# Kernel tuning notes

Measured on AMD Instinct MI355X. Metric: run time of the kernel, lower is better.

Reference implementation:

```python
import jax, jax.numpy as jnp
import numpy as np

B, L, D_IN, H, TAGS = 16, 128, 512, 256, 45


def setup_inputs() -> dict:
    key = jax.random.key(0)
    ks = jax.random.split(key, 10)
    s = 0.02
    return {
        "contextualized": jax.random.normal(ks[0], (B, L, D_IN), jnp.float32),
        "sentence_lengths": jax.random.randint(ks[1], (B,), 64, L + 1, jnp.int32),
        "desired_arcs": jax.random.randint(ks[2], (B, L), 0, L + 1, jnp.int32),
        "desired_labels": jax.random.randint(ks[3], (B, L), 0, TAGS, jnp.int32),
        "W1": jax.random.normal(ks[4], (D_IN, H), jnp.float32) * s,
        "b1": jnp.zeros((H,), jnp.float32),
        "root": jax.random.normal(ks[5], (H,), jnp.float32) * s,
        "Wp": jax.random.normal(ks[6], (2 * H, H), jnp.float32) * s,
        "bp": jnp.zeros((H,), jnp.float32),
        "W_arc": jax.random.normal(ks[7], (H, 1), jnp.float32) * s,
        "b_arc": jnp.zeros((1,), jnp.float32),
        "W_lab": jax.random.normal(ks[8], (H, TAGS), jnp.float32) * s,
        "b_lab": jnp.zeros((TAGS,), jnp.float32),
    }


def _forward(contextualized, sentence_lengths, desired_arcs, desired_labels,
             W1, b1, root, Wp, bp, W_arc, b_arc, W_lab, b_lab):
    b, l, _ = contextualized.shape
    h = W1.shape[1]
    # token representations: dense + relu
    hidden = jax.nn.relu(contextualized @ W1 + b1)                      # [B,L,H]
    # prepend learned root vector
    root_t = jnp.broadcast_to(root, (b, 1, h))
    cwr = jnp.concatenate([root_t, hidden], axis=1)                     # [B,L+1,H]
    # pairs dense: concat([tile_a, tile_b]) @ Wp == hidden@Wa + cwr@Wb (broadcast-add)
    Wa, Wb = Wp[:h], Wp[h:]
    pre = (hidden @ Wa)[:, :, None, :] + (cwr @ Wb)[:, None, :, :] + bp
    pairs_repr = jax.nn.relu(pre)                                       # [B,L,L+1,H]
    # valid-token mask from sentence lengths
    mask = (jnp.arange(l)[None, :] < sentence_lengths[:, None]).astype(jnp.float32)
    denom = jnp.maximum(mask.sum(), 1.0)
    # UAS: arc logits over L+1 head candidates, softmax CE vs gold arcs
    arc_logits = jnp.squeeze(pairs_repr @ W_arc, -1) + b_arc[0]         # [B,L,L+1]
    arc_logp = jax.nn.log_softmax(arc_logits, axis=-1)
    arc_ce = -jnp.take_along_axis(arc_logp, desired_arcs[:, :, None], axis=-1)[..., 0]
    uas_loss = jnp.sum(arc_ce * mask) / denom
    # LAS: select pair repr at gold arc, dense -> tag logits, softmax CE
    sel = jnp.take_along_axis(pairs_repr, desired_arcs[:, :, None, None].astype(jnp.int32)
                              .repeat(1, axis=2), axis=2)[:, :, 0, :]   # [B,L,H]
    label_logits = sel @ W_lab + b_lab                                  # [B,L,TAGS]
    lab_logp = jax.nn.log_softmax(label_logits, axis=-1)
    lab_ce = -jnp.take_along_axis(lab_logp, desired_labels[:, :, None], axis=-1)[..., 0]
    las_loss = jnp.sum(lab_ce * mask) / denom
    return (uas_loss + las_loss) * 0.5


def reference(contextualized, sentence_lengths, desired_arcs, desired_labels,
              W1, b1, root, Wp, bp, W_arc, b_arc, W_lab, b_lab):
    return _forward(contextualized, sentence_lengths, desired_arcs, desired_labels,
                    W1, b1, root, Wp, bp, W_arc, b_arc, W_lab, b_lab)
```

## Files before the change

### kernel.cpp

```cpp
#include <hip/hip_runtime.h>
#include <math.h>

#define NB 16
#define NL 128
#define DIN 512
#define NH 256
#define NTAGS 45
#define NM (NB*NL)
#define NJ (NL+1)

#define H_OFF     0
#define U_OFF     (2*NM*NH)
#define HV_OFF    (3*NM*NH)
#define VROOT_OFF (4*NM*NH)
#define ACC_OFF   (VROOT_OFF + NH)

__global__ __launch_bounds__(256) void gemm_hidden(
    const float* __restrict__ A,
    const float* __restrict__ W,
    const float* __restrict__ Wp,
    const float* __restrict__ root,
    float* __restrict__ h,
    float* __restrict__ vroot,
    float* __restrict__ accum)
{
    __shared__ float As[2][16][36];
    __shared__ float Bs[2][16][68];
    __shared__ float part[4][64];
    int m0 = blockIdx.x * 32;
    int n0 = blockIdx.y * 64;
    int kbase = blockIdx.z * 256;
    int tid = threadIdx.x;
    if (blockIdx.x == 0 && blockIdx.y == 0 && blockIdx.z == 0 && tid == 0) {
        accum[0] = 0.f;
        ((int*)accum)[1] = 0;
    }
    int lm = tid >> 2, lk = (tid & 3) * 4;
    int bk = tid >> 4, bn = (tid & 15) * 4;
    int tm = tid >> 4, tn = tid & 15;
    float acc[2][4] = {{0.f}};
    float4 a_r, b_r;

    auto LOADK = [&](int c) {
        int k0 = kbase + c * 16;
        if (tid < 128)
            a_r = *(const float4*)&A[(size_t)(m0 + lm) * DIN + k0 + lk];
        b_r = *(const float4*)&W[(size_t)(k0 + bk) * NH + n0 + bn];
    };
    auto WRITE = [&](int buf) {
        if (tid < 128) {
            As[buf][lk + 0][lm] = a_r.x; As[buf][lk + 1][lm] = a_r.y;
            As[buf][lk + 2][lm] = a_r.z; As[buf][lk + 3][lm] = a_r.w;
        }
        *(float4*)&Bs[buf][bk][bn] = b_r;
    };

    LOADK(0);
    WRITE(0);
    LOADK(1);
    __syncthreads();
    for (int c = 0; c < 16; ++c) {
        int buf = c & 1;
        #pragma unroll
        for (int kk = 0; kk < 16; kk++) {
            float2 a2 = *(const float2*)&As[buf][kk][tm * 2];
            float4 bv = *(const float4*)&Bs[buf][kk][tn * 4];
            float ar[2] = {a2.x, a2.y};
            float br[4] = {bv.x, bv.y, bv.z, bv.w};
            #pragma unroll
            for (int r = 0; r < 2; r++)
                #pragma unroll
                for (int cc = 0; cc < 4; cc++)
                    acc[r][cc] = fmaf(ar[r], br[cc], acc[r][cc]);
        }
        if (c < 15) {
            WRITE(buf ^ 1);
            if (c < 14) LOADK(c + 2);
            __syncthreads();
        }
    }
    float* hz = h + (size_t)blockIdx.z * NM * NH;
    int col = n0 + tn * 4;
    #pragma unroll
    for (int r = 0; r < 2; r++) {
        int row = m0 + tm * 2 + r;
        *(float4*)&hz[(size_t)row * NH + col] =
            make_float4(acc[r][0], acc[r][1], acc[r][2], acc[r][3]);
    }

    if (blockIdx.x == 63 && blockIdx.z == 1) {
        __syncthreads();
        int vcol = n0 + (tid & 63);
        int kc = tid >> 6;
        float p = 0.f;
        #pragma unroll 8
        for (int c = kc * 64; c < kc * 64 + 64; c++)
            p += root[c] * Wp[(size_t)(NH + c) * NH + vcol];
        part[kc][tid & 63] = p;
        __syncthreads();
        if (tid < 64)
            vroot[n0 + tid] = part[0][tid] + part[1][tid]
                            + part[2][tid] + part[3][tid];
    }
}

__global__ __launch_bounds__(256) void gemm_uv(
    const float* __restrict__ h,
    const float* __restrict__ b1,
    const float* __restrict__ Wp,
    const float* __restrict__ bp,
    float* __restrict__ u,
    float* __restrict__ hv)
{
    __shared__ float As[2][16][68];
    __shared__ float Bs[2][16][36];
    int m0 = blockIdx.x * 64;
    int n0 = blockIdx.y * 32;
    int tid = threadIdx.x;
    bool isU = (n0 < NH);
    int arow = tid >> 2, akq = (tid & 3) * 4;
    int bk = tid >> 3, bn = (tid & 7) * 4;
    int tm = tid >> 3, tn = tid & 7;
    float acc[2][4] = {{0.f}};
    float4 ha_r, hb_r, bi_r, b_r;

    auto LOADK = [&](int c) {
        int k0 = c * 16;
        size_t base = (size_t)(m0 + arow) * NH + k0 + akq;
        ha_r = *(const float4*)&h[base];
        hb_r = *(const float4*)&h[base + (size_t)NM * NH];
        bi_r = *(const float4*)&b1[k0 + akq];
        if (tid < 128) {
            int ck = k0 + bk;
            if (isU) b_r = *(const float4*)&Wp[(size_t)ck * NH + n0 + bn];
            else     b_r = *(const float4*)&Wp[(size_t)(NH + ck) * NH + (n0 - NH) + bn];
        }
    };
    auto WRITE = [&](int buf) {
        As[buf][akq + 0][arow] = fmaxf(ha_r.x + hb_r.x + bi_r.x, 0.f);
        As[buf][akq + 1][arow] = fmaxf(ha_r.y + hb_r.y + bi_r.y, 0.f);
        As[buf][akq + 2][arow] = fmaxf(ha_r.z + hb_r.z + bi_r.z, 0.f);
        As[buf][akq + 3][arow] = fmaxf(ha_r.w + hb_r.w + bi_r.w, 0.f);
        if (tid < 128)
            *(float4*)&Bs[buf][bk][bn] = b_r;
    };

    LOADK(0);
    WRITE(0);
    LOADK(1);
    __syncthreads();
    for (int c = 0; c < 16; ++c) {
        int buf = c & 1;
        #pragma unroll
        for (int kk = 0; kk < 16; kk++) {
            float2 a2 = *(const float2*)&As[buf][kk][tm * 2];
            float4 bv = *(const float4*)&Bs[buf][kk][tn * 4];
            float ar[2] = {a2.x, a2.y};
            float br[4] = {bv.x, bv.y, bv.z, bv.w};
            #pragma unroll
            for (int r = 0; r < 2; r++)
                #pragma unroll
                for (int cc = 0; cc < 4; cc++)
                    acc[r][cc] = fmaf(ar[r], br[cc], acc[r][cc]);
        }
        if (c < 15) {
            WRITE(buf ^ 1);
            if (c < 14) LOADK(c + 2);
            __syncthreads();
        }
    }
    if (isU) {
        int col = n0 + tn * 4;
        float4 bb = *(const float4*)&bp[col];
        #pragma unroll
        for (int r = 0; r < 2; r++) {
            int row = m0 + tm * 2 + r;
            *(float4*)&u[(size_t)row * NH + col] = make_float4(
                acc[r][0] + bb.x, acc[r][1] + bb.y,
                acc[r][2] + bb.z, acc[r][3] + bb.w);
        }
    } else {
        int col = (n0 - NH) + tn * 4;
        #pragma unroll
        for (int r = 0; r < 2; r++) {
            int row = m0 + tm * 2 + r;
            *(float4*)&hv[(size_t)row * NH + col] = make_float4(
                acc[r][0], acc[r][1], acc[r][2], acc[r][3]);
        }
    }
}

#define NBLK (NB*16)

__global__ __launch_bounds__(512) void score_loss_kernel(
    const float* __restrict__ u, const float* __restrict__ hv,
    const float* __restrict__ vroot, const float* __restrict__ W_arc,
    const float* __restrict__ W_lab, const float* __restrict__ b_lab,
    const int* __restrict__ slens, const int* __restrict__ arcs,
    const int* __restrict__ labels,
    float* __restrict__ accum, float* __restrict__ out)
{
    __shared__ float2 v2_s[128][130];
    __shared__ float2 u2_s[8][128];
    __shared__ float2 wa2_s[128];
    __shared__ float2 sel2_s[32][9];
    __shared__ float  ce_s[8];
    __shared__ int    arc_s[8], lab_s[8];

    int bb = blockIdx.x;
    int i0 = blockIdx.y * 8;
    int tid = threadIdx.x;
    int w = tid >> 6;
    int lane = tid & 63;
    int slen = slens[bb];

    if (i0 < slen) {
        {
            int r = tid >> 6, kq = (tid & 63) * 4;
            float4 a4 = *(const float4*)&u[(size_t)(bb * NL + i0 + r) * NH + kq];
            u2_s[r][(kq >> 1) + 0] = make_float2(a4.x, a4.y);
            u2_s[r][(kq >> 1) + 1] = make_float2(a4.z, a4.w);
        }
        if (tid < 128)
            wa2_s[tid] = *(const float2*)&W_arc[tid * 2];
        if (tid < 8) {
            int rg = bb * NL + i0 + tid;
            arc_s[tid] = arcs[rg];
            lab_s[tid] = labels[rg];
        }

        {
            int jo  = lane >> 4;
            int kf0 = lane & 15;
            #pragma unroll
            for (int sj = 0; sj < 4; ++sj) {
                int j = sj * 32 + w * 4 + jo;
                const float* src = hv + (size_t)(bb * NL + j) * NH;
                #pragma unroll
                for (int sk = 0; sk < 4; ++sk) {
                    int kf = sk * 16 + kf0;
                    float4 t4 = *(const float4*)&src[kf * 4];
                    v2_s[2 * kf + 0][j + 1] = make_float2(t4.x, t4.y);
                    v2_s[2 * kf + 1][j + 1] = make_float2(t4.z, t4.w);
                }
            }
            if (w == 0) {
                float4 t4 = *(const float4*)&vroot[lane * 4];
                v2_s[2 * lane + 0][0] = make_float2(t4.x, t4.y);
                v2_s[2 * lane + 1][0] = make_float2(t4.z, t4.w);
            }
        }
        __syncthreads();

        float acc1 = 0.f, acc2 = 0.f, s128 = 0.f, lacc = 0.f;
        int a = arc_s[w];

        __builtin_amdgcn_s_setprio(1);
        #pragma unroll
        for (int c = 0; c < 4; ++c) {
            int k0 = c * 64;
            int kb = k0 >> 1;
            const float2* urow = u2_s[w] + kb;
            const float2* warow = wa2_s + kb;

            #pragma unroll 8
            for (int kk2 = 0; kk2 < 32; ++kk2) {
                float2 u2 = urow[kk2];
                float2 w2 = warow[kk2];
                float4 q = *(const float4*)&v2_s[kb + kk2][2 * lane];
                acc1 += fmaxf(u2.x + q.x, 0.f) * w2.x
                      + fmaxf(u2.y + q.y, 0.f) * w2.y;
                acc2 += fmaxf(u2.x + q.z, 0.f) * w2.x
                      + fmaxf(u2.y + q.w, 0.f) * w2.y;
            }
            if (lane < 32) {
                float2 u2 = urow[lane];
                float2 w2 = warow[lane];
                float2 vv = v2_s[kb + lane][128];
                s128 += fmaxf(u2.x + vv.x, 0.f) * w2.x
                      + fmaxf(u2.y + vv.y, 0.f) * w2.y;
                float2 vs = v2_s[kb + lane][a];
                sel2_s[lane][w] = make_float2(fmaxf(u2.x + vs.x, 0.f),
                                              fmaxf(u2.y + vs.y, 0.f));
            }
            if (lane < NTAGS) {
                #pragma unroll 8
                for (int kk2 = 0; kk2 < 32; ++kk2) {
                    float2 s2 = sel2_s[kk2][w];
                    float w0 = W_lab[(size_t)(k0 + 2 * kk2) * NTAGS + lane];
                    float w1 = W_lab[(size_t)(k0 + 2 * kk2 + 1) * NTAGS + lane];
                    lacc = fmaf(s2.x, w0, fmaf(s2.y, w1, lacc));
                }
            }
        }
        __builtin_amdgcn_s_setprio(0);

        float s128t = s128;
        #pragma unroll
        for (int off = 32; off > 0; off >>= 1)
            s128t += __shfl_xor(s128t, off);
        float m = fmaxf(acc1, acc2);
        #pragma unroll
        for (int off = 32; off > 0; off >>= 1)
            m = fmaxf(m, __shfl_xor(m, off));
        m = fmaxf(m, s128t);
        float e = expf(acc1 - m) + expf(acc2 - m);
        #pragma unroll
        for (int off = 32; off > 0; off >>= 1)
            e += __shfl_xor(e, off);
        e += expf(s128t - m);
        float cand = (a & 1) ? acc2 : acc1;
        float s_a = __shfl(cand, (a >> 1) & 63, 64);
        if (a == 128) s_a = s128t;
        float arc_ce = (m + logf(e)) - s_a;

        float logit = (lane < NTAGS) ? (lacc + b_lab[lane]) : -INFINITY;
        float m2 = logit;
        #pragma unroll
        for (int off = 32; off > 0; off >>= 1)
            m2 = fmaxf(m2, __shfl_xor(m2, off));
        float e2 = (lane < NTAGS) ? expf(logit - m2) : 0.f;
        #pragma unroll
        for (int off = 32; off > 0; off >>= 1)
            e2 += __shfl_xor(e2, off);
        float l_t = __shfl(logit, lab_s[w], 64);
        float lab_ce = (m2 + logf(e2)) - l_t;

        float tot = ((i0 + w) < slen) ? (arc_ce + lab_ce) : 0.f;
        if (lane == 0) ce_s[w] = tot;
        __syncthreads();
        if (tid == 0)
            atomicAdd(accum, ce_s[0] + ce_s[1] + ce_s[2] + ce_s[3]
                           + ce_s[4] + ce_s[5] + ce_s[6] + ce_s[7]);
    }

    if (tid == 0) {
        __threadfence();
        int prev = atomicAdd((int*)accum + 1, 1);
        if (prev == NBLK - 1) {
            int d = 0;
            #pragma unroll
            for (int q = 0; q < NB; ++q) d += slens[q];
            float s = atomicAdd(accum, 0.f);
            out[0] = 0.5f * s / fmaxf((float)d, 1.f);
        }
    }
}

extern "C" void kernel_launch(void* const* d_in, const int* in_sizes, int n_in,
                              void* d_out, int out_size, void* d_ws, size_t ws_size,
                              hipStream_t stream) {
    (void)in_sizes; (void)n_in; (void)out_size; (void)ws_size;
    const float* ctx   = (const float*)d_in[0];
    const int*   slens = (const int*)  d_in[1];
    const int*   arcs  = (const int*)  d_in[2];
    const int*   labs  = (const int*)  d_in[3];
    const float* W1    = (const float*)d_in[4];
    const float* b1    = (const float*)d_in[5];
    const float* root  = (const float*)d_in[6];
    const float* Wp    = (const float*)d_in[7];
    const float* bp    = (const float*)d_in[8];
    const float* W_arc = (const float*)d_in[9];
    const float* W_lab = (const float*)d_in[11];
    const float* b_lab = (const float*)d_in[12];
    float* out = (float*)d_out;

    float* ws    = (float*)d_ws;
    float* h     = ws + H_OFF;
    float* u     = ws + U_OFF;
    float* hv    = ws + HV_OFF;
    float* vroot = ws + VROOT_OFF;
    float* accum = ws + ACC_OFF;

    gemm_hidden<<<dim3(64, 4, 2), 256, 0, stream>>>(ctx, W1, Wp, root, h, vroot, accum);
    gemm_uv<<<dim3(32, 16), 256, 0, stream>>>(h, b1, Wp, bp, u, hv);
    score_loss_kernel<<<dim3(NB, 16), 512, 0, stream>>>(
        u, hv, vroot, W_arc, W_lab, b_lab, slens, arcs, labs, accum, out);
}
```

Baseline: 128.3 us.

## Split hidden-dim reduction across two wave groups in score kernel

```diff
diff --git a/kernel.cpp b/kernel.cpp
--- a/kernel.cpp
+++ b/kernel.cpp
@@ -192,7 +192,7 @@
 
 #define NBLK (NB*16)
 
-__global__ __launch_bounds__(512) void score_loss_kernel(
+__global__ __launch_bounds__(1024) void score_loss_kernel(
     const float* __restrict__ u, const float* __restrict__ hv,
     const float* __restrict__ vroot, const float* __restrict__ W_arc,
     const float* __restrict__ W_lab, const float* __restrict__ b_lab,
@@ -203,23 +203,26 @@
     __shared__ float2 v2_s[128][130];
     __shared__ float2 u2_s[8][128];
     __shared__ float2 wa2_s[128];
-    __shared__ float2 sel2_s[32][9];
+    __shared__ float2 sel2_s[32][17];
+    __shared__ float4 pair_s[8][64];
     __shared__ float  ce_s[8];
     __shared__ int    arc_s[8], lab_s[8];
 
     int bb = blockIdx.x;
     int i0 = blockIdx.y * 8;
     int tid = threadIdx.x;
-    int w = tid >> 6;
+    int w16 = tid >> 6;
     int lane = tid & 63;
+    int r  = w16 & 7;
+    int kh = w16 >> 3;
     int slen = slens[bb];
 
     if (i0 < slen) {
-        {
-            int r = tid >> 6, kq = (tid & 63) * 4;
-            float4 a4 = *(const float4*)&u[(size_t)(bb * NL + i0 + r) * NH + kq];
-            u2_s[r][(kq >> 1) + 0] = make_float2(a4.x, a4.y);
-            u2_s[r][(kq >> 1) + 1] = make_float2(a4.z, a4.w);
+        if (tid < 512) {
+            int rr = tid >> 6, kq = (tid & 63) * 4;
+            float4 a4 = *(const float4*)&u[(size_t)(bb * NL + i0 + rr) * NH + kq];
+            u2_s[rr][(kq >> 1) + 0] = make_float2(a4.x, a4.y);
+            u2_s[rr][(kq >> 1) + 1] = make_float2(a4.z, a4.w);
         }
         if (tid < 128)
             wa2_s[tid] = *(const float2*)&W_arc[tid * 2];
@@ -233,8 +236,8 @@
             int jo  = lane >> 4;
             int kf0 = lane & 15;
             #pragma unroll
-            for (int sj = 0; sj < 4; ++sj) {
-                int j = sj * 32 + w * 4 + jo;
+            for (int sj = 0; sj < 2; ++sj) {
+                int j = sj * 64 + w16 * 4 + jo;
                 const float* src = hv + (size_t)(bb * NL + j) * NH;
                 #pragma unroll
                 for (int sk = 0; sk < 4; ++sk) {
@@ -244,7 +247,7 @@
                     v2_s[2 * kf + 1][j + 1] = make_float2(t4.z, t4.w);
                 }
             }
-            if (w == 0) {
+            if (w16 == 0) {
                 float4 t4 = *(const float4*)&vroot[lane * 4];
                 v2_s[2 * lane + 0][0] = make_float2(t4.x, t4.y);
                 v2_s[2 * lane + 1][0] = make_float2(t4.z, t4.w);
@@ -253,14 +256,15 @@
         __syncthreads();
 
         float acc1 = 0.f, acc2 = 0.f, s128 = 0.f, lacc = 0.f;
-        int a = arc_s[w];
+        int a = arc_s[r];
 
         __builtin_amdgcn_s_setprio(1);
         #pragma unroll
-        for (int c = 0; c < 4; ++c) {
+        for (int cc = 0; cc < 2; ++cc) {
+            int c = kh * 2 + cc;
             int k0 = c * 64;
             int kb = k0 >> 1;
-            const float2* urow = u2_s[w] + kb;
+            const float2* urow = u2_s[r] + kb;
             const float2* warow = wa2_s + kb;
 
             #pragma unroll 8
@@ -280,13 +284,13 @@
                 s128 += fmaxf(u2.x + vv.x, 0.f) * w2.x
                       + fmaxf(u2.y + vv.y, 0.f) * w2.y;
                 float2 vs = v2_s[kb + lane][a];
-                sel2_s[lane][w] = make_float2(fmaxf(u2.x + vs.x, 0.f),
-                                              fmaxf(u2.y + vs.y, 0.f));
+                sel2_s[lane][w16] = make_float2(fmaxf(u2.x + vs.x, 0.f),
+                                                fmaxf(u2.y + vs.y, 0.f));
             }
             if (lane < NTAGS) {
                 #pragma unroll 8
                 for (int kk2 = 0; kk2 < 32; ++kk2) {
-                    float2 s2 = sel2_s[kk2][w];
+                    float2 s2 = sel2_s[kk2][w16];
                     float w0 = W_lab[(size_t)(k0 + 2 * kk2) * NTAGS + lane];
                     float w1 = W_lab[(size_t)(k0 + 2 * kk2 + 1) * NTAGS + lane];
                     lacc = fmaf(s2.x, w0, fmaf(s2.y, w1, lacc));
@@ -295,39 +299,48 @@
         }
         __builtin_amdgcn_s_setprio(0);
 
-        float s128t = s128;
-        #pragma unroll
-        for (int off = 32; off > 0; off >>= 1)
-            s128t += __shfl_xor(s128t, off);
-        float m = fmaxf(acc1, acc2);
-        #pragma unroll
-        for (int off = 32; off > 0; off >>= 1)
-            m = fmaxf(m, __shfl_xor(m, off));
-        m = fmaxf(m, s128t);
-        float e = expf(acc1 - m) + expf(acc2 - m);
-        #pragma unroll
-        for (int off = 32; off > 0; off >>= 1)
-            e += __shfl_xor(e, off);
-        e += expf(s128t - m);
-        float cand = (a & 1) ? acc2 : acc1;
-        float s_a = __shfl(cand, (a >> 1) & 63, 64);
-        if (a == 128) s_a = s128t;
-        float arc_ce = (m + logf(e)) - s_a;
-
-        float logit = (lane < NTAGS) ? (lacc + b_lab[lane]) : -INFINITY;
-        float m2 = logit;
-        #pragma unroll
-        for (int off = 32; off > 0; off >>= 1)
-            m2 = fmaxf(m2, __shfl_xor(m2, off));
-        float e2 = (lane < NTAGS) ? expf(logit - m2) : 0.f;
-        #pragma unroll
-        for (int off = 32; off > 0; off >>= 1)
-            e2 += __shfl_xor(e2, off);
-        float l_t = __shfl(logit, lab_s[w], 64);
-        float lab_ce = (m2 + logf(e2)) - l_t;
-
-        float tot = ((i0 + w) < slen) ? (arc_ce + lab_ce) : 0.f;
-        if (lane == 0) ce_s[w] = tot;
+        if (kh == 1)
+            pair_s[r][lane] = make_float4(acc1, acc2, s128, lacc);
+        __syncthreads();
+
+        if (kh == 0) {
+            float4 p = pair_s[r][lane];
+            acc1 += p.x; acc2 += p.y; s128 += p.z; lacc += p.w;
+
+            float s128t = s128;
+            #pragma unroll
+            for (int off = 32; off > 0; off >>= 1)
+                s128t += __shfl_xor(s128t, off);
+            float m = fmaxf(acc1, acc2);
+            #pragma unroll
+            for (int off = 32; off > 0; off >>= 1)
+                m = fmaxf(m, __shfl_xor(m, off));
+            m = fmaxf(m, s128t);
+            float e = expf(acc1 - m) + expf(acc2 - m);
+            #pragma unroll
+            for (int off = 32; off > 0; off >>= 1)
+                e += __shfl_xor(e, off);
+            e += expf(s128t - m);
+            float cand = (a & 1) ? acc2 : acc1;
+            float s_a = __shfl(cand, (a >> 1) & 63, 64);
+            if (a == 128) s_a = s128t;
+            float arc_ce = (m + logf(e)) - s_a;
+
+            float logit = (lane < NTAGS) ? (lacc + b_lab[lane]) : -INFINITY;
+            float m2 = logit;
+            #pragma unroll
+            for (int off = 32; off > 0; off >>= 1)
+                m2 = fmaxf(m2, __shfl_xor(m2, off));
+            float e2 = (lane < NTAGS) ? expf(logit - m2) : 0.f;
+            #pragma unroll
+            for (int off = 32; off > 0; off >>= 1)
+                e2 += __shfl_xor(e2, off);
+            float l_t = __shfl(logit, lab_s[r], 64);
+            float lab_ce = (m2 + logf(e2)) - l_t;
+
+            float tot = ((i0 + r) < slen) ? (arc_ce + lab_ce) : 0.f;
+            if (lane == 0) ce_s[r] = tot;
+        }
         __syncthreads();
         if (tid == 0)
             atomicAdd(accum, ce_s[0] + ce_s[1] + ce_s[2] + ce_s[3]
@@ -374,6 +387,6 @@
 
     gemm_hidden<<<dim3(64, 4, 2), 256, 0, stream>>>(ctx, W1, Wp, root, h, vroot, accum);
     gemm_uv<<<dim3(32, 16), 256, 0, stream>>>(h, b1, Wp, bp, u, hv);
-    score_loss_kernel<<<dim3(NB, 16), 512, 0, stream>>>(
+    score_loss_kernel<<<dim3(NB, 16), 1024, 0, stream>>>(
         u, hv, vroot, W_arc, W_lab, b_lab, slens, arcs, labs, accum, out);
 }
```

New measurement: 128.4 us. No clear change (+0.1%).

## Fuse three kernels into one cooperative persistent kernel with grid syncs

Applied to the files above, without the earlier changes.

```diff
diff --git a/kernel.cpp b/kernel.cpp
--- a/kernel.cpp
+++ b/kernel.cpp
@@ -1,5 +1,8 @@
 #include <hip/hip_runtime.h>
+#include <hip/hip_cooperative_groups.h>
 #include <math.h>
+
+namespace cg = cooperative_groups;
 
 #define NB 16
 #define NL 128
@@ -15,335 +18,340 @@
 #define VROOT_OFF (4*NM*NH)
 #define ACC_OFF   (VROOT_OFF + NH)
 
-__global__ __launch_bounds__(256) void gemm_hidden(
+#define SMEM_BYTES 145408
+
+__global__ __launch_bounds__(512) void fused_kernel(
     const float* __restrict__ A,
-    const float* __restrict__ W,
+    const float* __restrict__ W1,
     const float* __restrict__ Wp,
     const float* __restrict__ root,
-    float* __restrict__ h,
-    float* __restrict__ vroot,
-    float* __restrict__ accum)
+    const float* __restrict__ b1,
+    const float* __restrict__ bp,
+    const float* __restrict__ W_arc,
+    const float* __restrict__ W_lab,
+    const float* __restrict__ b_lab,
+    const int* __restrict__ slens, const int* __restrict__ arcs,
+    const int* __restrict__ labels,
+    float* __restrict__ h, float* __restrict__ u, float* __restrict__ hv,
+    float* __restrict__ vroot, float* __restrict__ accum,
+    float* __restrict__ out)
 {
-    __shared__ float As[2][16][36];
-    __shared__ float Bs[2][16][68];
-    __shared__ float part[4][64];
-    int m0 = blockIdx.x * 32;
-    int n0 = blockIdx.y * 64;
-    int kbase = blockIdx.z * 256;
+    __shared__ __align__(16) char smem[SMEM_BYTES];
+    cg::grid_group grid = cg::this_grid();
+    int B = blockIdx.x;
     int tid = threadIdx.x;
-    if (blockIdx.x == 0 && blockIdx.y == 0 && blockIdx.z == 0 && tid == 0) {
-        accum[0] = 0.f;
-        ((int*)accum)[1] = 0;
-    }
-    int lm = tid >> 2, lk = (tid & 3) * 4;
-    int bk = tid >> 4, bn = (tid & 15) * 4;
-    int tm = tid >> 4, tn = tid & 15;
-    float acc[2][4] = {{0.f}};
-    float4 a_r, b_r;
-
-    auto LOADK = [&](int c) {
-        int k0 = kbase + c * 16;
-        if (tid < 128)
-            a_r = *(const float4*)&A[(size_t)(m0 + lm) * DIN + k0 + lk];
-        b_r = *(const float4*)&W[(size_t)(k0 + bk) * NH + n0 + bn];
-    };
-    auto WRITE = [&](int buf) {
-        if (tid < 128) {
-            As[buf][lk + 0][lm] = a_r.x; As[buf][lk + 1][lm] = a_r.y;
-            As[buf][lk + 2][lm] = a_r.z; As[buf][lk + 3][lm] = a_r.w;
-        }
-        *(float4*)&Bs[buf][bk][bn] = b_r;
-    };
-
-    LOADK(0);
-    WRITE(0);
-    LOADK(1);
-    __syncthreads();
-    for (int c = 0; c < 16; ++c) {
-        int buf = c & 1;
-        #pragma unroll
-        for (int kk = 0; kk < 16; kk++) {
-            float2 a2 = *(const float2*)&As[buf][kk][tm * 2];
-            float4 bv = *(const float4*)&Bs[buf][kk][tn * 4];
-            float ar[2] = {a2.x, a2.y};
-            float br[4] = {bv.x, bv.y, bv.z, bv.w};
-            #pragma unroll
-            for (int r = 0; r < 2; r++)
+    int sub = tid >> 8;
+    int stid = tid & 255;
+
+    if (B == 0 && tid == 0) accum[0] = 0.f;
+
+    {
+        float* As_ = (float*)smem + sub * 3328;
+        float* Bs_ = As_ + 1152;
+        int t = B * 2 + sub;
+        int m0 = (t & 63) * 32;
+        int n0 = ((t >> 6) & 3) * 64;
+        int z  = t >> 8;
+        int kbase = z * 256;
+
+        int lm = stid >> 2, lk = (stid & 3) * 4;
+        int bk = stid >> 4, bn = (stid & 15) * 4;
+        int tm = stid >> 4, tn = stid & 15;
+        float acc[2][4] = {{0.f}};
+        float4 a_r, b_r;
+
+        auto LOADK = [&](int c) {
+            int k0 = kbase + c * 16;
+            if (stid < 128)
+                a_r = *(const float4*)&A[(size_t)(m0 + lm) * DIN + k0 + lk];
+            b_r = *(const float4*)&W1[(size_t)(k0 + bk) * NH + n0 + bn];
+        };
+        auto WRITE = [&](int buf) {
+            if (stid < 128) {
+                As_[buf*576 + (lk+0)*36 + lm] = a_r.x;
+                As_[buf*576 + (lk+1)*36 + lm] = a_r.y;
+                As_[buf*576 + (lk+2)*36 + lm] = a_r.z;
+                As_[buf*576 + (lk+3)*36 + lm] = a_r.w;
+            }
+            *(float4*)&Bs_[buf*1088 + bk*68 + bn] = b_r;
+        };
+
+        LOADK(0);
+        WRITE(0);
+        LOADK(1);
+        __syncthreads();
+        for (int c = 0; c < 16; ++c) {
+            int buf = c & 1;
+            #pragma unroll
+            for (int kk = 0; kk < 16; kk++) {
+                float2 a2 = *(const float2*)&As_[buf*576 + kk*36 + tm*2];
+                float4 bv = *(const float4*)&Bs_[buf*1088 + kk*68 + tn*4];
+                float ar[2] = {a2.x, a2.y};
+                float br[4] = {bv.x, bv.y, bv.z, bv.w};
                 #pragma unroll
-                for (int cc = 0; cc < 4; cc++)
-                    acc[r][cc] = fmaf(ar[r], br[cc], acc[r][cc]);
-        }
-        if (c < 15) {
-            WRITE(buf ^ 1);
-            if (c < 14) LOADK(c + 2);
-            __syncthreads();
-        }
-    }
-    float* hz = h + (size_t)blockIdx.z * NM * NH;
-    int col = n0 + tn * 4;
-    #pragma unroll
-    for (int r = 0; r < 2; r++) {
-        int row = m0 + tm * 2 + r;
-        *(float4*)&hz[(size_t)row * NH + col] =
-            make_float4(acc[r][0], acc[r][1], acc[r][2], acc[r][3]);
-    }
-
-    if (blockIdx.x == 63 && blockIdx.z == 1) {
-        __syncthreads();
-        int vcol = n0 + (tid & 63);
-        int kc = tid >> 6;
-        float p = 0.f;
-        #pragma unroll 8
-        for (int c = kc * 64; c < kc * 64 + 64; c++)
-            p += root[c] * Wp[(size_t)(NH + c) * NH + vcol];
-        part[kc][tid & 63] = p;
-        __syncthreads();
-        if (tid < 64)
-            vroot[n0 + tid] = part[0][tid] + part[1][tid]
-                            + part[2][tid] + part[3][tid];
-    }
-}
-
-__global__ __launch_bounds__(256) void gemm_uv(
-    const float* __restrict__ h,
-    const float* __restrict__ b1,
-    const float* __restrict__ Wp,
-    const float* __restrict__ bp,
-    float* __restrict__ u,
-    float* __restrict__ hv)
-{
-    __shared__ float As[2][16][68];
-    __shared__ float Bs[2][16][36];
-    int m0 = blockIdx.x * 64;
-    int n0 = blockIdx.y * 32;
-    int tid = threadIdx.x;
-    bool isU = (n0 < NH);
-    int arow = tid >> 2, akq = (tid & 3) * 4;
-    int bk = tid >> 3, bn = (tid & 7) * 4;
-    int tm = tid >> 3, tn = tid & 7;
-    float acc[2][4] = {{0.f}};
-    float4 ha_r, hb_r, bi_r, b_r;
-
-    auto LOADK = [&](int c) {
-        int k0 = c * 16;
-        size_t base = (size_t)(m0 + arow) * NH + k0 + akq;
-        ha_r = *(const float4*)&h[base];
-        hb_r = *(const float4*)&h[base + (size_t)NM * NH];
-        bi_r = *(const float4*)&b1[k0 + akq];
-        if (tid < 128) {
-            int ck = k0 + bk;
-            if (isU) b_r = *(const float4*)&Wp[(size_t)ck * NH + n0 + bn];
-            else     b_r = *(const float4*)&Wp[(size_t)(NH + ck) * NH + (n0 - NH) + bn];
-        }
-    };
-    auto WRITE = [&](int buf) {
-        As[buf][akq + 0][arow] = fmaxf(ha_r.x + hb_r.x + bi_r.x, 0.f);
-        As[buf][akq + 1][arow] = fmaxf(ha_r.y + hb_r.y + bi_r.y, 0.f);
-        As[buf][akq + 2][arow] = fmaxf(ha_r.z + hb_r.z + bi_r.z, 0.f);
-        As[buf][akq + 3][arow] = fmaxf(ha_r.w + hb_r.w + bi_r.w, 0.f);
-        if (tid < 128)
-            *(float4*)&Bs[buf][bk][bn] = b_r;
-    };
-
-    LOADK(0);
-    WRITE(0);
-    LOADK(1);
-    __syncthreads();
-    for (int c = 0; c < 16; ++c) {
-        int buf = c & 1;
-        #pragma unroll
-        for (int kk = 0; kk < 16; kk++) {
-            float2 a2 = *(const float2*)&As[buf][kk][tm * 2];
-            float4 bv = *(const float4*)&Bs[buf][kk][tn * 4];
-            float ar[2] = {a2.x, a2.y};
-            float br[4] = {bv.x, bv.y, bv.z, bv.w};
-            #pragma unroll
-            for (int r = 0; r < 2; r++)
-                #pragma unroll
-                for (int cc = 0; cc < 4; cc++)
-                    acc[r][cc] = fmaf(ar[r], br[cc], acc[r][cc]);
-        }
-        if (c < 15) {
-            WRITE(buf ^ 1);
-            if (c < 14) LOADK(c + 2);
-            __syncthreads();
-        }
-    }
-    if (isU) {
+                for (int r = 0; r < 2; r++)
+                    #pragma unroll
+                    for (int cc = 0; cc < 4; cc++)
+                        acc[r][cc] = fmaf(ar[r], br[cc], acc[r][cc]);
+            }
+            if (c < 15) {
+                WRITE(buf ^ 1);
+                if (c < 14) LOADK(c + 2);
+                __syncthreads();
+            }
+        }
+        float* hz = h + (size_t)z * NM * NH;
         int col = n0 + tn * 4;
-        float4 bb = *(const float4*)&bp[col];
         #pragma unroll
         for (int r = 0; r < 2; r++) {
             int row = m0 + tm * 2 + r;
-            *(float4*)&u[(size_t)row * NH + col] = make_float4(
-                acc[r][0] + bb.x, acc[r][1] + bb.y,
-                acc[r][2] + bb.z, acc[r][3] + bb.w);
-        }
-    } else {
-        int col = (n0 - NH) + tn * 4;
-        #pragma unroll
-        for (int r = 0; r < 2; r++) {
-            int row = m0 + tm * 2 + r;
-            *(float4*)&hv[(size_t)row * NH + col] = make_float4(
-                acc[r][0], acc[r][1], acc[r][2], acc[r][3]);
-        }
+            *(float4*)&hz[(size_t)row * NH + col] =
+                make_float4(acc[r][0], acc[r][1], acc[r][2], acc[r][3]);
+        }
+
+        bool q = ((t & 63) == 63) && (z == 1);
+        float* part_ = (float*)(smem + 26624) + sub * 256;
+        float p = 0.f;
+        int vcol = n0 + (stid & 63);
+        int kc = stid >> 6;
+        if (q) {
+            #pragma unroll 8
+            for (int c = kc * 64; c < kc * 64 + 64; c++)
+                p += root[c] * Wp[(size_t)(NH + c) * NH + vcol];
+        }
+        __syncthreads();
+        if (q) part_[kc * 64 + (stid & 63)] = p;
+        __syncthreads();
+        if (q && stid < 64)
+            vroot[n0 + stid] = part_[0*64+stid] + part_[1*64+stid]
+                             + part_[2*64+stid] + part_[3*64+stid];
     }
-}
-
-#define NBLK (NB*16)
-
-__global__ __launch_bounds__(512) void score_loss_kernel(
-    const float* __restrict__ u, const float* __restrict__ hv,
-    const float* __restrict__ vroot, const float* __restrict__ W_arc,
-    const float* __restrict__ W_lab, const float* __restrict__ b_lab,
-    const int* __restrict__ slens, const int* __restrict__ arcs,
-    const int* __restrict__ labels,
-    float* __restrict__ accum, float* __restrict__ out)
-{
-    __shared__ float2 v2_s[128][130];
-    __shared__ float2 u2_s[8][128];
-    __shared__ float2 wa2_s[128];
-    __shared__ float2 sel2_s[32][9];
-    __shared__ float  ce_s[8];
-    __shared__ int    arc_s[8], lab_s[8];
-
-    int bb = blockIdx.x;
-    int i0 = blockIdx.y * 8;
-    int tid = threadIdx.x;
-    int w = tid >> 6;
-    int lane = tid & 63;
-    int slen = slens[bb];
-
-    if (i0 < slen) {
-        {
-            int r = tid >> 6, kq = (tid & 63) * 4;
-            float4 a4 = *(const float4*)&u[(size_t)(bb * NL + i0 + r) * NH + kq];
-            u2_s[r][(kq >> 1) + 0] = make_float2(a4.x, a4.y);
-            u2_s[r][(kq >> 1) + 1] = make_float2(a4.z, a4.w);
-        }
-        if (tid < 128)
-            wa2_s[tid] = *(const float2*)&W_arc[tid * 2];
-        if (tid < 8) {
-            int rg = bb * NL + i0 + tid;
-            arc_s[tid] = arcs[rg];
-            lab_s[tid] = labels[rg];
-        }
-
-        {
-            int jo  = lane >> 4;
-            int kf0 = lane & 15;
-            #pragma unroll
-            for (int sj = 0; sj < 4; ++sj) {
-                int j = sj * 32 + w * 4 + jo;
-                const float* src = hv + (size_t)(bb * NL + j) * NH;
+    grid.sync();
+
+    {
+        float* As_ = (float*)smem + sub * 3328;
+        float* Bs_ = As_ + 2176;
+        int t = B * 2 + sub;
+        int m0 = (t & 31) * 64;
+        int n0 = (t >> 5) * 32;
+        bool isU = (n0 < NH);
+
+        int arow = stid >> 2, akq = (stid & 3) * 4;
+        int bk = stid >> 3, bn = (stid & 7) * 4;
+        int tm = stid >> 3, tn = stid & 7;
+        float acc[2][4] = {{0.f}};
+        float4 ha_r, hb_r, bi_r, b_r;
+
+        auto LOADK = [&](int c) {
+            int k0 = c * 16;
+            size_t base = (size_t)(m0 + arow) * NH + k0 + akq;
+            ha_r = *(const float4*)&h[base];
+            hb_r = *(const float4*)&h[base + (size_t)NM * NH];
+            bi_r = *(const float4*)&b1[k0 + akq];
+            if (stid < 128) {
+                int ck = k0 + bk;
+                if (isU) b_r = *(const float4*)&Wp[(size_t)ck * NH + n0 + bn];
+                else     b_r = *(const float4*)&Wp[(size_t)(NH + ck) * NH + (n0 - NH) + bn];
+            }
+        };
+        auto WRITE = [&](int buf) {
+            As_[buf*1088 + (akq+0)*68 + arow] = fmaxf(ha_r.x + hb_r.x + bi_r.x, 0.f);
+            As_[buf*1088 + (akq+1)*68 + arow] = fmaxf(ha_r.y + hb_r.y + bi_r.y, 0.f);
+            As_[buf*1088 + (akq+2)*68 + arow] = fmaxf(ha_r.z + hb_r.z + bi_r.z, 0.f);
+            As_[buf*1088 + (akq+3)*68 + arow] = fmaxf(ha_r.w + hb_r.w + bi_r.w, 0.f);
+            if (stid < 128)
+                *(float4*)&Bs_[buf*576 + bk*36 + bn] = b_r;
+        };
+
+        LOADK(0);
+        WRITE(0);
+        LOADK(1);
+        __syncthreads();
+        for (int c = 0; c < 16; ++c) {
+            int buf = c & 1;
+            #pragma unroll
+            for (int kk = 0; kk < 16; kk++) {
+                float2 a2 = *(const float2*)&As_[buf*1088 + kk*68 + tm*2];
+                float4 bv = *(const float4*)&Bs_[buf*576 + kk*36 + tn*4];
+                float ar[2] = {a2.x, a2.y};
+                float br[4] = {bv.x, bv.y, bv.z, bv.w};
                 #pragma unroll
-                for (int sk = 0; sk < 4; ++sk) {
-                    int kf = sk * 16 + kf0;
-                    float4 t4 = *(const float4*)&src[kf * 4];
-                    v2_s[2 * kf + 0][j + 1] = make_float2(t4.x, t4.y);
-                    v2_s[2 * kf + 1][j + 1] = make_float2(t4.z, t4.w);
-                }
-            }
-            if (w == 0) {
-                float4 t4 = *(const float4*)&vroot[lane * 4];
-                v2_s[2 * lane + 0][0] = make_float2(t4.x, t4.y);
-                v2_s[2 * lane + 1][0] = make_float2(t4.z, t4.w);
-            }
-        }
-        __syncthreads();
-
-        float acc1 = 0.f, acc2 = 0.f, s128 = 0.f, lacc = 0.f;
-        int a = arc_s[w];
-
-        __builtin_amdgcn_s_setprio(1);
-        #pragma unroll
-        for (int c = 0; c < 4; ++c) {
-            int k0 = c * 64;
-            int kb = k0 >> 1;
-            const float2* urow = u2_s[w] + kb;
-            const float2* warow = wa2_s + kb;
-
-            #pragma unroll 8
-            for (int kk2 = 0; kk2 < 32; ++kk2) {
-                float2 u2 = urow[kk2];
-                float2 w2 = warow[kk2];
-                float4 q = *(const float4*)&v2_s[kb + kk2][2 * lane];
-                acc1 += fmaxf(u2.x + q.x, 0.f) * w2.x
-                      + fmaxf(u2.y + q.y, 0.f) * w2.y;
-                acc2 += fmaxf(u2.x + q.z, 0.f) * w2.x
-                      + fmaxf(u2.y + q.w, 0.f) * w2.y;
-            }
-            if (lane < 32) {
-                float2 u2 = urow[lane];
-                float2 w2 = warow[lane];
-                float2 vv = v2_s[kb + lane][128];
-                s128 += fmaxf(u2.x + vv.x, 0.f) * w2.x
-                      + fmaxf(u2.y + vv.y, 0.f) * w2.y;
-                float2 vs = v2_s[kb + lane][a];
-                sel2_s[lane][w] = make_float2(fmaxf(u2.x + vs.x, 0.f),
-                                              fmaxf(u2.y + vs.y, 0.f));
-            }
-            if (lane < NTAGS) {
+                for (int r = 0; r < 2; r++)
+                    #pragma unroll
+                    for (int cc = 0; cc < 4; cc++)
+                        acc[r][cc] = fmaf(ar[r], br[cc], acc[r][cc]);
+            }
+            if (c < 15) {
+                WRITE(buf ^ 1);
+                if (c < 14) LOADK(c + 2);
+                __syncthreads();
+            }
+        }
+        if (isU) {
+            int col = n0 + tn * 4;
+            float4 bb = *(const float4*)&bp[col];
+            #pragma unroll
+            for (int r = 0; r < 2; r++) {
+                int row = m0 + tm * 2 + r;
+                *(float4*)&u[(size_t)row * NH + col] = make_float4(
+                    acc[r][0] + bb.x, acc[r][1] + bb.y,
+                    acc[r][2] + bb.z, acc[r][3] + bb.w);
+            }
+        } else {
+            int col = (n0 - NH) + tn * 4;
+            #pragma unroll
+            for (int r = 0; r < 2; r++) {
+                int row = m0 + tm * 2 + r;
+                *(float4*)&hv[(size_t)row * NH + col] = make_float4(
+                    acc[r][0], acc[r][1], acc[r][2], acc[r][3]);
+            }
+        }
+    }
+    grid.sync();
+
+    {
+        float2* v2   = (float2*)smem;
+        float2* u2   = (float2*)(smem + 133120);
+        float2* wa2  = (float2*)(smem + 141312);
+        float2* sel2 = (float2*)(smem + 142336);
+        float*  ce_s = (float*)(smem + 144640);
+        int*    arc_s = (int*)(smem + 144672);
+        int*    lab_s = arc_s + 8;
+
+        int bb = B >> 4;
+        int i0 = (B & 15) * 8;
+        int w = tid >> 6;
+        int lane = tid & 63;
+        int slen = slens[bb];
+
+        if (i0 < slen) {
+            {
+                int r = tid >> 6, kq = (tid & 63) * 4;
+                float4 a4 = *(const float4*)&u[(size_t)(bb * NL + i0 + r) * NH + kq];
+                u2[r*128 + (kq >> 1) + 0] = make_float2(a4.x, a4.y);
+                u2[r*128 + (kq >> 1) + 1] = make_float2(a4.z, a4.w);
+            }
+            if (tid < 128)
+                wa2[tid] = *(const float2*)&W_arc[tid * 2];
+            if (tid < 8) {
+                int rg = bb * NL + i0 + tid;
+                arc_s[tid] = arcs[rg];
+                lab_s[tid] = labels[rg];
+            }
+
+            {
+                int jo  = lane >> 4;
+                int kf0 = lane & 15;
+                #pragma unroll
+                for (int sj = 0; sj < 4; ++sj) {
+                    int j = sj * 32 + w * 4 + jo;
+                    const float* src = hv + (size_t)(bb * NL + j) * NH;
+                    #pragma unroll
+                    for (int sk = 0; sk < 4; ++sk) {
+                        int kf = sk * 16 + kf0;
+                        float4 t4 = *(const float4*)&src[kf * 4];
+                        v2[(2*kf + 0)*130 + j + 1] = make_float2(t4.x, t4.y);
+                        v2[(2*kf + 1)*130 + j + 1] = make_float2(t4.z, t4.w);
+                    }
+                }
+                if (w == 0) {
+                    float4 t4 = *(const float4*)&vroot[lane * 4];
+                    v2[(2*lane + 0)*130 + 0] = make_float2(t4.x, t4.y);
+                    v2[(2*lane + 1)*130 + 0] = make_float2(t4.z, t4.w);
+                }
+            }
+            __syncthreads();
+
+            float acc1 = 0.f, acc2 = 0.f, s128 = 0.f, lacc = 0.f;
+            int a = arc_s[w];
+
+            __builtin_amdgcn_s_setprio(1);
+            #pragma unroll
+            for (int c = 0; c < 4; ++c) {
+                int k0 = c * 64;
+                int kb = k0 >> 1;
+                const float2* urow = u2 + w*128 + kb;
+                const float2* warow = wa2 + kb;
+
                 #pragma unroll 8
                 for (int kk2 = 0; kk2 < 32; ++kk2) {
-                    float2 s2 = sel2_s[kk2][w];
-                    float w0 = W_lab[(size_t)(k0 + 2 * kk2) * NTAGS + lane];
-                    float w1 = W_lab[(size_t)(k0 + 2 * kk2 + 1) * NTAGS + lane];
-                    lacc = fmaf(s2.x, w0, fmaf(s2.y, w1, lacc));
-                }
-            }
-        }
-        __builtin_amdgcn_s_setprio(0);
-
-        float s128t = s128;
+                    float2 u2v = urow[kk2];
+                    float2 w2v = warow[kk2];
+                    float4 q = *(const float4*)&v2[(kb + kk2)*130 + 2*lane];
+                    acc1 += fmaxf(u2v.x + q.x, 0.f) * w2v.x
+                          + fmaxf(u2v.y + q.y, 0.f) * w2v.y;
+                    acc2 += fmaxf(u2v.x + q.z, 0.f) * w2v.x
+                          + fmaxf(u2v.y + q.w, 0.f) * w2v.y;
+                }
+                if (lane < 32) {
+                    float2 u2v = urow[lane];
+                    float2 w2v = warow[lane];
+                    float2 vv = v2[(kb + lane)*130 + 128];
+                    s128 += fmaxf(u2v.x + vv.x, 0.f) * w2v.x
+                          + fmaxf(u2v.y + vv.y, 0.f) * w2v.y;
+                    float2 vs = v2[(kb + lane)*130 + a];
+                    sel2[lane*9 + w] = make_float2(fmaxf(u2v.x + vs.x, 0.f),
+                                                   fmaxf(u2v.y + vs.y, 0.f));
+                }
+                if (lane < NTAGS) {
+                    #pragma unroll 8
+                    for (int kk2 = 0; kk2 < 32; ++kk2) {
+                        float2 s2 = sel2[kk2*9 + w];
+                        float w0 = W_lab[(size_t)(k0 + 2*kk2) * NTAGS + lane];
+                        float w1 = W_lab[(size_t)(k0 + 2*kk2 + 1) * NTAGS + lane];
+                        lacc = fmaf(s2.x, w0, fmaf(s2.y, w1, lacc));
+                    }
+                }
+            }
+            __builtin_amdgcn_s_setprio(0);
+
+            float s128t = s128;
+            #pragma unroll
+            for (int off = 32; off > 0; off >>= 1)
+                s128t += __shfl_xor(s128t, off);
+            float m = fmaxf(acc1, acc2);
+            #pragma unroll
+            for (int off = 32; off > 0; off >>= 1)
+                m = fmaxf(m, __shfl_xor(m, off));
+            m = fmaxf(m, s128t);
+            float e = expf(acc1 - m) + expf(acc2 - m);
+            #pragma unroll
+            for (int off = 32; off > 0; off >>= 1)
+                e += __shfl_xor(e, off);
+            e += expf(s128t - m);
+            float cand = (a & 1) ? acc2 : acc1;
+            float s_a = __shfl(cand, (a >> 1) & 63, 64);
+            if (a == 128) s_a = s128t;
+            float arc_ce = (m + logf(e)) - s_a;
+
+            float logit = (lane < NTAGS) ? (lacc + b_lab[lane]) : -INFINITY;
+            float m2 = logit;
+            #pragma unroll
+            for (int off = 32; off > 0; off >>= 1)
+                m2 = fmaxf(m2, __shfl_xor(m2, off));
+            float e2 = (lane < NTAGS) ? expf(logit - m2) : 0.f;
+            #pragma unroll
+            for (int off = 32; off > 0; off >>= 1)
+                e2 += __shfl_xor(e2, off);
+            float l_t = __shfl(logit, lab_s[w], 64);
+            float lab_ce = (m2 + logf(e2)) - l_t;
+
+            float tot = ((i0 + w) < slen) ? (arc_ce + lab_ce) : 0.f;
+            if (lane == 0) ce_s[w] = tot;
+            __syncthreads();
+            if (tid == 0)
+                atomicAdd(accum, ce_s[0] + ce_s[1] + ce_s[2] + ce_s[3]
+                               + ce_s[4] + ce_s[5] + ce_s[6] + ce_s[7]);
+        }
+    }
+    grid.sync();
+
+    if (B == 0 && tid == 0) {
+        int d = 0;
         #pragma unroll
-        for (int off = 32; off > 0; off >>= 1)
-            s128t += __shfl_xor(s128t, off);
-        float m = fmaxf(acc1, acc2);
-        #pragma unroll
-        for (int off = 32; off > 0; off >>= 1)
-            m = fmaxf(m, __shfl_xor(m, off));
-        m = fmaxf(m, s128t);
-        float e = expf(acc1 - m) + expf(acc2 - m);
-        #pragma unroll
-        for (int off = 32; off > 0; off >>= 1)
-            e += __shfl_xor(e, off);
-        e += expf(s128t - m);
-        float cand = (a & 1) ? acc2 : acc1;
-        float s_a = __shfl(cand, (a >> 1) & 63, 64);
-        if (a == 128) s_a = s128t;
-        float arc_ce = (m + logf(e)) - s_a;
-
-        float logit = (lane < NTAGS) ? (lacc + b_lab[lane]) : -INFINITY;
-        float m2 = logit;
-        #pragma unroll
-        for (int off = 32; off > 0; off >>= 1)
-            m2 = fmaxf(m2, __shfl_xor(m2, off));
-        float e2 = (lane < NTAGS) ? expf(logit - m2) : 0.f;
-        #pragma unroll
-        for (int off = 32; off > 0; off >>= 1)
-            e2 += __shfl_xor(e2, off);
-        float l_t = __shfl(logit, lab_s[w], 64);
-        float lab_ce = (m2 + logf(e2)) - l_t;
-
-        float tot = ((i0 + w) < slen) ? (arc_ce + lab_ce) : 0.f;
-        if (lane == 0) ce_s[w] = tot;
-        __syncthreads();
-        if (tid == 0)
-            atomicAdd(accum, ce_s[0] + ce_s[1] + ce_s[2] + ce_s[3]
-                           + ce_s[4] + ce_s[5] + ce_s[6] + ce_s[7]);
-    }
-
-    if (tid == 0) {
-        __threadfence();
-        int prev = atomicAdd((int*)accum + 1, 1);
-        if (prev == NBLK - 1) {
-            int d = 0;
-            #pragma unroll
-            for (int q = 0; q < NB; ++q) d += slens[q];
-            float s = atomicAdd(accum, 0.f);
-            out[0] = 0.5f * s / fmaxf((float)d, 1.f);
-        }
+        for (int q = 0; q < NB; ++q) d += slens[q];
+        float s = atomicAdd(accum, 0.f);
+        out[0] = 0.5f * s / fmaxf((float)d, 1.f);
     }
 }
 
@@ -372,8 +380,13 @@
     float* vroot = ws + VROOT_OFF;
     float* accum = ws + ACC_OFF;
 
-    gemm_hidden<<<dim3(64, 4, 2), 256, 0, stream>>>(ctx, W1, Wp, root, h, vroot, accum);
-    gemm_uv<<<dim3(32, 16), 256, 0, stream>>>(h, b1, Wp, bp, u, hv);
-    score_loss_kernel<<<dim3(NB, 16), 512, 0, stream>>>(
-        u, hv, vroot, W_arc, W_lab, b_lab, slens, arcs, labs, accum, out);
+    void* args[] = {
+        (void*)&ctx, (void*)&W1, (void*)&Wp, (void*)&root,
+        (void*)&b1, (void*)&bp, (void*)&W_arc, (void*)&W_lab, (void*)&b_lab,
+        (void*)&slens, (void*)&arcs, (void*)&labs,
+        (void*)&h, (void*)&u, (void*)&hv, (void*)&vroot, (void*)&accum,
+        (void*)&out
+    };
+    hipLaunchCooperativeKernel((const void*)fused_kernel, dim3(256), dim3(512),
+                               args, 0, stream);
 }
```

Measured after the change: 222.4 us. 1.73x slower.
